# Kernel tuning notes

Measured on AMD Instinct MI355X. Metric: run time of the kernel, lower is better.

## Reference

```python
import jax, jax.numpy as jnp
import numpy as np

NEG = -1e30  # finite stand-in for -inf (keeps logsumexp NaN-free)
B, T, V, L = 64, 1024, 512, 128
BLANK = 0


def setup_inputs() -> dict:
    key = jax.random.key(0)
    k1, k2 = jax.random.split(key)
    outputs = jax.random.normal(k1, (B, T, V), dtype=jnp.float32)
    labels = jax.random.randint(k2, (B, L), 1, V, dtype=jnp.int32)  # labels avoid blank=0
    output_lengths = jnp.full((B,), T, dtype=jnp.int32)
    label_lengths = jnp.full((B,), L, dtype=jnp.int32)
    return {"outputs": outputs, "labels": labels,
            "output_lengths": output_lengths, "label_lengths": label_lengths}


def _ctc_loss(log_probs, labels, output_lengths, label_lengths):
    # log_probs: [B, T, V]; labels: [B, L]
    S = 2 * L + 1
    # extended label sequence: blank, l1, blank, l2, ..., blank
    ext = jnp.full((B, S), BLANK, dtype=labels.dtype).at[:, 1::2].set(labels)
    # skip transition allowed at s if ext[s] != blank and ext[s] != ext[s-2]
    ext_m2 = jnp.pad(ext, ((0, 0), (2, 0)), constant_values=BLANK)[:, :S]
    skip = (ext != BLANK) & (ext != ext_m2) & (jnp.arange(S) >= 2)

    # emission log-probs on the lattice: emit[b, t, s] = log_probs[b, t, ext[b, s]]
    bidx = jnp.arange(B)
    emit = log_probs[bidx[:, None, None], jnp.arange(T)[None, :, None], ext[:, None, :]]  # [B,T,S]
    emit_t = jnp.moveaxis(emit, 1, 0)  # [T, B, S]

    alpha0 = (jnp.full((B, S), NEG, dtype=log_probs.dtype)
              .at[:, 0].set(emit_t[0, :, 0])
              .at[:, 1].set(emit_t[0, :, 1]))

    neg1 = jnp.full((B, 1), NEG, dtype=log_probs.dtype)
    neg2 = jnp.full((B, 2), NEG, dtype=log_probs.dtype)

    def step(alpha, e):
        p0 = alpha
        p1 = jnp.concatenate([neg1, alpha[:, :-1]], axis=1)
        p2 = jnp.where(skip, jnp.concatenate([neg2, alpha[:, :-2]], axis=1), NEG)
        m = jnp.maximum(p0, jnp.maximum(p1, p2))
        lse = m + jnp.log(jnp.exp(p0 - m) + jnp.exp(p1 - m) + jnp.exp(p2 - m))
        new = lse + e
        return new, new

    _, alphas = jax.lax.scan(step, alpha0, emit_t[1:])
    alphas = jnp.concatenate([alpha0[None], alphas], axis=0)  # [T, B, S]

    a_last = alphas[output_lengths - 1, bidx]  # [B, S] alpha at final frame per sample
    s1 = 2 * label_lengths      # final blank state
    s0 = 2 * label_lengths - 1  # final label state
    a0 = a_last[bidx, s0]
    a1 = a_last[bidx, s1]
    m = jnp.maximum(a0, a1)
    log_lik = m + jnp.log(jnp.exp(a0 - m) + jnp.exp(a1 - m))
    # reduction='mean': per-sample nll divided by target length, then batch mean
    loss = -log_lik / label_lengths.astype(log_lik.dtype)
    return jnp.mean(loss)


def reference(outputs, labels, output_lengths, label_lengths):
    return _ctc_loss(outputs, labels, output_lengths, label_lengths)
```

## Files before the change

### kernel.cpp

```cpp
#include <hip/hip_runtime.h>

#define B_ 64
#define T_ 1024
#define V_ 512
#define L_ 128
#define LOG2E_ 1.4426950408889634f
#define LN2_   0.6931471805599453f
#define C_ 56
#define RW4_ 65
#define NC_ ((T_ - 1 + C_ - 1) / C_)

typedef float f4_t __attribute__((ext_vector_type(4)));

__device__ __forceinline__ float exp2_fast(float x) { return __builtin_amdgcn_exp2f(x); }
__device__ __forceinline__ float log2_fast(float x) { return __builtin_amdgcn_logf(x); }
__device__ __forceinline__ float ldx(float v, int e) { return __builtin_amdgcn_ldexpf(v, e); }

__device__ __forceinline__ float dpp_shr1_f(float x) {
    return __int_as_float(__builtin_amdgcn_update_dpp(0, __float_as_int(x), 0x138, 0xf, 0xf, true));
}
__device__ __forceinline__ int dpp_shr1_i(int x) {
    return __builtin_amdgcn_update_dpp(0, x, 0x138, 0xf, 0xf, true);
}

__global__ __launch_bounds__(512, 1) void ctc_alpha_kernel(
    const float* __restrict__ outputs, const int* __restrict__ labels,
    const int* __restrict__ out_lens, const int* __restrict__ lab_lens,
    float* __restrict__ ws, float* __restrict__ out)
{
    const int b    = blockIdx.x;
    const int tid  = threadIdx.x;
    const int wid  = tid >> 6;
    const int lane = tid & 63;

    int* cnt = (int*)ws;
    float* losses = ws + 16;

    __shared__ f4_t  ring4[2][C_ * RW4_];
    __shared__ f4_t  scr[7][2][129];
    __shared__ float save2[2];
    __shared__ int   saveE[2];
    __shared__ int   amLast;

    const int olen  = out_lens[b];
    const int ll    = lab_lens[b];
    const int s0q   = 2 * ll - 1;
    const int s1q   = 2 * ll;
    const int tlast = olen - 1;
    const int l0  = s0q >> 2, j0 = s0q & 3;
    const int l1e = (s1q == 256) ? 63 : (s1q >> 2);
    const int j1  = s1q & 3;
    const float* base = outputs + (size_t)b * T_ * V_;
    const int*   lab  = labels + b * L_;

    const int cA = lab[2 * lane];
    const int cB = lab[2 * lane + 1];

    float sk1 = 0.f, sk3 = 0.f;
    float v0 = 0.f, v1 = 0.f, v2 = 0.f, v3 = 0.f, vx = 0.f;
    int   E = 0;
    const bool isl0 = (lane == 0);
    if (wid == 0) {
        __builtin_amdgcn_s_setprio(3);
        sk3 = (cB != cA) ? 1.f : 0.f;
        if (lane >= 1) sk1 = (cA != lab[2 * lane - 1]) ? 1.f : 0.f;
        if (isl0) {
            v0 = exp2_fast(base[0]      * LOG2E_);
            v1 = exp2_fast(base[lab[0]] * LOG2E_);
        }
        if (tlast == 0) {
            float w0 = (j0==0)?v0:(j0==1)?v1:(j0==2)?v2:v3;
            float w1 = (s1q==256) ? vx : ((j1==0)?v0:(j1==1)?v1:(j1==2)?v2:v3);
            if (lane == l0)  { save2[0] = w0; saveE[0] = E; }
            if (lane == l1e) { save2[1] = w1; saveE[1] = E; }
        }
    } else {
        __builtin_amdgcn_s_setprio(0);
    }

    auto produce = [&](int bb, int t0) {
        const int w1 = wid - 1;
        f4_t A[8], Cc[8];
        #pragma unroll
        for (int m = 0; m < 8; ++m) {
            int t = t0 + w1 + 7 * m;
            const f4_t* rp = (const f4_t*)((t < T_) ? (base + (size_t)t * V_) : base);
            A[m]  = rp[lane];
            Cc[m] = rp[lane + 64];
        }
        scr[w1][0][lane]      = A[0];
        scr[w1][0][lane + 64] = Cc[0];
        #pragma unroll
        for (int m = 1; m <= 8; ++m) {
            if (m < 8) {
                scr[w1][m & 1][lane]      = A[m];
                scr[w1][m & 1][lane + 64] = Cc[m];
            }
            int r = w1 + 7 * (m - 1);
            int t = t0 + r;
            if (t < T_) {
                const float* sf = (const float*)&scr[w1][(m - 1) & 1][0];
                float gb = sf[0];
                float g1 = sf[cA];
                float g3 = sf[cB];
                f4_t e;
                e.x = exp2_fast(gb * LOG2E_);
                e.y = exp2_fast(g1 * LOG2E_);
                e.z = exp2_fast(g3 * LOG2E_);
                e.w = 0.f;
                ring4[bb][r * RW4_ + lane] = e;
            }
        }
    };

    auto step = [&](f4_t e) {
        float up1 = dpp_shr1_f(v3);
        int   upE = dpp_shr1_i(E);
        upE = isl0 ? E : upE;

        int d    = upE - E;
        int mpos = (d > 0) ? d : 0;
        int sin  = (d < 0) ? d : 0;
        int sown = -mpos;
        E += mpos;
        v0 = ldx(v0, sown); v1 = ldx(v1, sown); v2 = ldx(v2, sown);
        v3 = ldx(v3, sown); vx = ldx(vx, sown);
        up1 = ldx(up1, sin);

        float n0 = (v0 + up1) * e.x;
        float n1 = fmaf(sk1, up1, v1 + v0) * e.y;
        float n2 = (v2 + v1) * e.x;
        float n3 = fmaf(sk3, v1, v3 + v2) * e.z;
        vx = (vx + v3) * e.x;
        v0 = n0; v1 = n1; v2 = n2; v3 = n3;
    };

    auto renorm = [&]() {
        float mx = fmaxf(fmaxf(v0, v1), fmaxf(v2, v3));
        mx = fmaxf(mx, vx);
        int ex = (__float_as_int(mx) >> 23) - 126;
        v0 = ldx(v0, -ex); v1 = ldx(v1, -ex); v2 = ldx(v2, -ex); v3 = ldx(v3, -ex);
        vx = ldx(vx, -ex);
        E += ex;
    };

    auto consume = [&](int bb, int t0) {
        const f4_t* rp4 = &ring4[bb][lane];
        f4_t eb2[2];
        eb2[0] = rp4[0];
        eb2[1] = rp4[RW4_];

        bool chk = (t0 + C_ > T_) || ((unsigned)(tlast - t0) < (unsigned)C_);
        if (!chk) {
            #pragma unroll 8
            for (int r = 0; r < C_; ++r) {
                f4_t e = eb2[r & 1];
                if (r + 2 < C_) eb2[r & 1] = rp4[(r + 2) * RW4_];
                step(e);
                if ((r & 3) == 3) renorm();
            }
        } else {
            #pragma unroll 4
            for (int r = 0; r < C_; ++r) {
                int t = t0 + r;
                if (t >= T_) break;
                f4_t e = eb2[r & 1];
                if (r + 2 < C_) eb2[r & 1] = rp4[(r + 2) * RW4_];
                step(e);
                if ((r & 3) == 3) renorm();
                if (t == tlast) {
                    float w0 = (j0==0)?v0:(j0==1)?v1:(j0==2)?v2:v3;
                    float w1 = (s1q==256) ? vx : ((j1==0)?v0:(j1==1)?v1:(j1==2)?v2:v3);
                    if (lane == l0)  { save2[0] = w0; saveE[0] = E; }
                    if (lane == l1e) { save2[1] = w1; saveE[1] = E; }
                }
            }
        }
    };

    if (wid > 0) produce(0, 1);
    __syncthreads();
    for (int c = 0; c < NC_; ++c) {
        if (wid > 0) {
            if (c + 1 < NC_) produce((c + 1) & 1, 1 + (c + 1) * C_);
        } else {
            consume(c & 1, 1 + c * C_);
        }
        __syncthreads();
    }

    if (tid == 0) {
        float lx = log2_fast(save2[0]) + (float)saveE[0];
        float ly = log2_fast(save2[1]) + (float)saveE[1];
        float m  = fmaxf(lx, ly);
        float lik2 = m + log2_fast(exp2_fast(lx - m) + exp2_fast(ly - m));
        float loss = -(lik2 * LN2_) / (float)ll;
        __hip_atomic_store(&losses[b], loss, __ATOMIC_RELAXED, __HIP_MEMORY_SCOPE_AGENT);
        int old = __hip_atomic_fetch_add(cnt, 1, __ATOMIC_ACQ_REL, __HIP_MEMORY_SCOPE_AGENT);
        amLast = (old == B_ - 1);
    }
    __syncthreads();
    if (amLast && wid == 0) {
        float v = __hip_atomic_load(&losses[lane], __ATOMIC_RELAXED, __HIP_MEMORY_SCOPE_AGENT);
        #pragma unroll
        for (int o = 32; o > 0; o >>= 1) v += __shfl_down(v, o);
        if (lane == 0) out[0] = v * (1.0f / B_);
    }
}

extern "C" void kernel_launch(void* const* d_in, const int* in_sizes, int n_in,
                              void* d_out, int out_size, void* d_ws, size_t ws_size,
                              hipStream_t stream) {
    const float* outputs  = (const float*)d_in[0];
    const int*   labels   = (const int*)d_in[1];
    const int*   out_lens = (const int*)d_in[2];
    const int*   lab_lens = (const int*)d_in[3];

    (void)hipMemsetAsync(d_ws, 0, 64, stream);
    ctc_alpha_kernel<<<B_, 512, 0, stream>>>(outputs, labels, out_lens, lab_lens,
                                             (float*)d_ws, (float*)d_out);
}
```

Before: 224.6 us.

## Prefetch producer loads two chunks ahead and trim the serial alpha step

Producer waves now split loading from packing. They keep two register buffer sets so the global loads for chunk c+2 are issued before chunk c+1 is packed into LDS, hiding more load latency. The consumer wave's recurrence step now applies the exponent shift to the three emission values instead of rescaling all five state registers. A DPP variant that keeps the old value in lane 0 removes the lane-0 select. The consumer prefetch depth from LDS rises from 2 to 8 rows, and the blank emission is taken with readfirstlane instead of an LDS read. The cost is many more producer VGPRs for the double register buffers.

Measured after the change: 230.4 us. 1.03x slower.

```diff
diff --git a/kernel.cpp b/kernel.cpp
--- a/kernel.cpp
+++ b/kernel.cpp
@@ -19,8 +19,11 @@
 __device__ __forceinline__ float dpp_shr1_f(float x) {
     return __int_as_float(__builtin_amdgcn_update_dpp(0, __float_as_int(x), 0x138, 0xf, 0xf, true));
 }
-__device__ __forceinline__ int dpp_shr1_i(int x) {
-    return __builtin_amdgcn_update_dpp(0, x, 0x138, 0xf, 0xf, true);
+__device__ __forceinline__ int dpp_shr1_keep_i(int old, int x) {
+    return __builtin_amdgcn_update_dpp(old, x, 0x138, 0xf, 0xf, false);
+}
+__device__ __forceinline__ float bcast_first_f(float x) {
+    return __int_as_float(__builtin_amdgcn_readfirstlane(__float_as_int(x)));
 }
 
 __global__ __launch_bounds__(512, 1) void ctc_alpha_kernel(
@@ -78,9 +81,10 @@
         __builtin_amdgcn_s_setprio(0);
     }
 
-    auto produce = [&](int bb, int t0) {
+    f4_t A0[8], C0r[8], A1[8], C1r[8];
+
+    auto pload = [&](f4_t (&A)[8], f4_t (&Cc)[8], int t0) {
         const int w1 = wid - 1;
-        f4_t A[8], Cc[8];
         #pragma unroll
         for (int m = 0; m < 8; ++m) {
             int t = t0 + w1 + 7 * m;
@@ -88,6 +92,9 @@
             A[m]  = rp[lane];
             Cc[m] = rp[lane + 64];
         }
+    };
+    auto ppack = [&](int bb, f4_t (&A)[8], f4_t (&Cc)[8], int t0) {
+        const int w1 = wid - 1;
         scr[w1][0][lane]      = A[0];
         scr[w1][0][lane + 64] = Cc[0];
         #pragma unroll
@@ -99,8 +106,8 @@
             int r = w1 + 7 * (m - 1);
             int t = t0 + r;
             if (t < T_) {
+                float gb = bcast_first_f(A[m - 1].x);
                 const float* sf = (const float*)&scr[w1][(m - 1) & 1][0];
-                float gb = sf[0];
                 float g1 = sf[cA];
                 float g3 = sf[cB];
                 f4_t e;
@@ -115,23 +122,20 @@
 
     auto step = [&](f4_t e) {
         float up1 = dpp_shr1_f(v3);
-        int   upE = dpp_shr1_i(E);
-        upE = isl0 ? E : upE;
-
+        int   upE = dpp_shr1_keep_i(E, E);
         int d    = upE - E;
         int mpos = (d > 0) ? d : 0;
-        int sin  = (d < 0) ? d : 0;
         int sown = -mpos;
         E += mpos;
-        v0 = ldx(v0, sown); v1 = ldx(v1, sown); v2 = ldx(v2, sown);
-        v3 = ldx(v3, sown); vx = ldx(vx, sown);
-        up1 = ldx(up1, sin);
-
-        float n0 = (v0 + up1) * e.x;
-        float n1 = fmaf(sk1, up1, v1 + v0) * e.y;
-        float n2 = (v2 + v1) * e.x;
-        float n3 = fmaf(sk3, v1, v3 + v2) * e.z;
-        vx = (vx + v3) * e.x;
+        up1 = ldx(up1, d);
+        float ex_ = ldx(e.x, sown);
+        float ey_ = ldx(e.y, sown);
+        float ez_ = ldx(e.z, sown);
+        float n0 = (v0 + up1) * ex_;
+        float n1 = fmaf(sk1, up1, v1 + v0) * ey_;
+        float n2 = (v2 + v1) * ex_;
+        float n3 = fmaf(sk3, v1, v3 + v2) * ez_;
+        vx = (vx + v3) * ex_;
         v0 = n0; v1 = n1; v2 = n2; v3 = n3;
     };
 
@@ -146,16 +150,16 @@
 
     auto consume = [&](int bb, int t0) {
         const f4_t* rp4 = &ring4[bb][lane];
-        f4_t eb2[2];
-        eb2[0] = rp4[0];
-        eb2[1] = rp4[RW4_];
+        f4_t eb8[8];
+        #pragma unroll
+        for (int i = 0; i < 8; ++i) eb8[i] = rp4[i * RW4_];
 
         bool chk = (t0 + C_ > T_) || ((unsigned)(tlast - t0) < (unsigned)C_);
         if (!chk) {
             #pragma unroll 8
             for (int r = 0; r < C_; ++r) {
-                f4_t e = eb2[r & 1];
-                if (r + 2 < C_) eb2[r & 1] = rp4[(r + 2) * RW4_];
+                f4_t e = eb8[r & 7];
+                if (r + 8 < C_) eb8[r & 7] = rp4[(r + 8) * RW4_];
                 step(e);
                 if ((r & 3) == 3) renorm();
             }
@@ -164,8 +168,8 @@
             for (int r = 0; r < C_; ++r) {
                 int t = t0 + r;
                 if (t >= T_) break;
-                f4_t e = eb2[r & 1];
-                if (r + 2 < C_) eb2[r & 1] = rp4[(r + 2) * RW4_];
+                f4_t e = eb8[r & 7];
+                if (r + 8 < C_) eb8[r & 7] = rp4[(r + 8) * RW4_];
                 step(e);
                 if ((r & 3) == 3) renorm();
                 if (t == tlast) {
@@ -178,11 +182,22 @@
         }
     };
 
-    if (wid > 0) produce(0, 1);
+    if (wid > 0) {
+        pload(A0, C0r, 1);
+        ppack(0, A0, C0r, 1);
+        if (NC_ > 1) pload(A1, C1r, 1 + C_);
+    }
     __syncthreads();
     for (int c = 0; c < NC_; ++c) {
         if (wid > 0) {
-            if (c + 1 < NC_) produce((c + 1) & 1, 1 + (c + 1) * C_);
+            if (c + 2 < NC_) {
+                if ((c + 2) & 1) pload(A1, C1r, 1 + (c + 2) * C_);
+                else             pload(A0, C0r, 1 + (c + 2) * C_);
+            }
+            if (c + 1 < NC_) {
+                if ((c + 1) & 1) ppack(1, A1, C1r, 1 + (c + 1) * C_);
+                else             ppack(0, A0, C0r, 1 + (c + 1) * C_);
+            }
         } else {
             consume(c & 1, 1 + c * C_);
         }
```
